# Kernel optimization log

Hardware: AMD Instinct MI355X
Metric: run time of the kernel (lower is better)

## Reference

```python
import jax, jax.numpy as jnp
import numpy as np

# Module hyperparameters (from init_kwargs)
B, D = 512, 65536        # input: [B, D]
Q = 64                   # sub-vectors per sample
R = 8                    # number of independent KMeans problems
L = 64                   # clusters (codebook size) per problem
ITERS = 10               # KMeans max_iter
SUBD = D // Q            # sub-vector dim = 1024
N = B * Q // R           # points per KMeans problem = 4096


def setup_inputs() -> dict:
    key = jax.random.key(0)
    x = jax.random.normal(key, (B, D), dtype=jnp.float32)
    return {"x": x}


def _kmeans(pts):
    """Batched Lloyd's KMeans. pts: [R, N, d]. Returns (labels [R,N], centers [R,L,d])."""
    # init: random distinct points per group (torch_kmeans 'rnd' init)
    key = jax.random.key(42)
    init_idx = jax.vmap(lambda k: jax.random.permutation(k, N)[:L])(
        jax.random.split(key, R))                          # [R, L]
    centers = jax.vmap(lambda p, i: p[i])(pts, init_idx)   # [R, L, d]
    x2 = jnp.sum(pts * pts, axis=-1, keepdims=True)        # [R, N, 1]

    def assign(centers):
        c2 = jnp.sum(centers * centers, axis=-1)           # [R, L]
        d2 = x2 + c2[:, None, :] - 2.0 * jnp.einsum('rnd,rld->rnl', pts, centers)
        return jnp.argmin(d2, axis=-1)                     # [R, N]

    def step(centers, _):
        labels = assign(centers)
        onehot = jax.nn.one_hot(labels, L, dtype=pts.dtype)      # [R, N, L]
        counts = jnp.sum(onehot, axis=1)                          # [R, L]
        sums = jnp.einsum('rnl,rnd->rld', onehot, pts)            # [R, L, d]
        new_c = jnp.where(counts[..., None] > 0,
                          sums / jnp.maximum(counts[..., None], 1.0),
                          centers)                                # keep empty clusters
        return new_c, None

    centers, _ = jax.lax.scan(step, centers, None, length=ITERS)
    labels = assign(centers)
    return labels, centers


def _quantize(x):
    orig_shape = x.shape
    pts = x.reshape(B, Q, SUBD).reshape(R, N, SUBD)        # [R, N, d/q]
    labels, centers = _kmeans(pts)
    # gather: replace each point by its centroid
    xq = jax.vmap(lambda c, lab: c[lab])(centers, labels)  # [R, N, d/q]
    return xq.reshape(orig_shape)


def reference(x):
    # FedLite_Layer.forward in training mode
    return _quantize(x)
```

## Files before the change

kernel.cpp:

```cpp
#include <hip/hip_runtime.h>
#include <stdint.h>
#include <stddef.h>


#define JAX_PARTITIONABLE 1

static constexpr int R_    = 8;
static constexpr int N_    = 4096;
static constexpr int L_    = 64;
static constexpr int D_    = 1024;
static constexpr int ITERS = 10;
static constexpr int ROWS  = R_ * N_;
static constexpr int SEGS  = 8;

__device__ __forceinline__ unsigned rotl32(unsigned x, int r) {
  return (x << r) | (x >> (32 - r));
}

__device__ __forceinline__ void tf2x32(unsigned k0, unsigned k1,
                                       unsigned c0, unsigned c1,
                                       unsigned &o0, unsigned &o1) {
  unsigned ks2 = k0 ^ k1 ^ 0x1BD11BDAu;
  unsigned x0 = c0 + k0, x1 = c1 + k1;
#define TF_R4(a,b,c,d) { x0 += x1; x1 = rotl32(x1,a); x1 ^= x0; \
                         x0 += x1; x1 = rotl32(x1,b); x1 ^= x0; \
                         x0 += x1; x1 = rotl32(x1,c); x1 ^= x0; \
                         x0 += x1; x1 = rotl32(x1,d); x1 ^= x0; }
  TF_R4(13,15,26,6);  x0 += k1;  x1 += ks2 + 1u;
  TF_R4(17,29,16,24); x0 += ks2; x1 += k0  + 2u;
  TF_R4(13,15,26,6);  x0 += k0;  x1 += k1  + 3u;
  TF_R4(17,29,16,24); x0 += k1;  x1 += ks2 + 4u;
  TF_R4(13,15,26,6);  x0 += ks2; x1 += k0  + 5u;
#undef TF_R4
  o0 = x0; o1 = x1;
}

__device__ __forceinline__ void jax_split2(unsigned k0, unsigned k1,
                                           unsigned &nk0, unsigned &nk1,
                                           unsigned &sk0, unsigned &sk1) {
#if JAX_PARTITIONABLE
  tf2x32(k0, k1, 0u, 0u, nk0, nk1);
  tf2x32(k0, k1, 0u, 1u, sk0, sk1);
#else
  unsigned a0, a1, b0, b1;
  tf2x32(k0, k1, 0u, 2u, a0, a1);
  tf2x32(k0, k1, 1u, 3u, b0, b1);
  nk0 = a0; nk1 = b0; sk0 = a1; sk1 = b1;
#endif
}

__global__ __launch_bounds__(1024) void k_rng_x2(const float* __restrict__ pts,
                                                 float* __restrict__ x2,
                                                 int* __restrict__ init_idx) {
  __shared__ unsigned long long arr[N_];
  __shared__ unsigned short perm[N_];
  const int t = threadIdx.x;

  if (blockIdx.x >= R_) {
    const int row = (blockIdx.x - R_) * 16 + (t >> 6);
    const int lane = t & 63;
    const float4* P = (const float4*)(pts + (size_t)row * D_);
    float s = 0.f;
#pragma unroll
    for (int i = 0; i < 4; ++i) {
      float4 v = P[lane + 64 * i];
      s += v.x * v.x + v.y * v.y + v.z * v.z + v.w * v.w;
    }
#pragma unroll
    for (int m = 32; m > 0; m >>= 1) s += __shfl_down(s, m);
    if (lane == 0) x2[row] = s;
    return;
  }

  const int r = blockIdx.x;

  unsigned k0, k1;
#if JAX_PARTITIONABLE
  tf2x32(0u, 42u, 0u, (unsigned)r, k0, k1);
#else
  {
    unsigned a0, a1, b0, b1;
    unsigned i0 = 2u * r, i1 = 2u * r + 1u;
    if (r < 4) { tf2x32(0u, 42u, i0, i0 + 8u, a0, a1); tf2x32(0u, 42u, i1, i1 + 8u, b0, b1); k0 = a0; k1 = b0; }
    else       { tf2x32(0u, 42u, i0 - 8u, i0, a0, a1); tf2x32(0u, 42u, i1 - 8u, i1, b0, b1); k0 = a1; k1 = b1; }
  }
#endif

  for (int i = t; i < N_; i += 1024) perm[i] = (unsigned short)i;
  __syncthreads();

  for (int round = 0; round < 2; ++round) {
    unsigned nk0, nk1, sk0, sk1;
    jax_split2(k0, k1, nk0, nk1, sk0, sk1);
    for (int j = t; j < N_; j += 1024) {
      unsigned o0, o1, skey;
#if JAX_PARTITIONABLE
      tf2x32(sk0, sk1, 0u, (unsigned)j, o0, o1);
      skey = o0 ^ o1;
#else
      if (j < 2048) { tf2x32(sk0, sk1, (unsigned)j, (unsigned)(j + 2048), o0, o1); skey = o0; }
      else          { tf2x32(sk0, sk1, (unsigned)(j - 2048), (unsigned)j, o0, o1); skey = o1; }
#endif
      arr[j] = ((unsigned long long)skey << 24) |
               ((unsigned long long)(unsigned)j << 12) |
               (unsigned long long)perm[j];
    }
    __syncthreads();
    for (int k = 2; k <= N_; k <<= 1) {
      for (int j2 = k >> 1; j2 >= 1; j2 >>= 1) {
        for (int q = t; q < N_ / 2; q += 1024) {
          int low = q & (j2 - 1);
          int i0 = ((q ^ low) << 1) | low;
          int i1 = i0 | j2;
          bool up = ((i0 & k) == 0);
          unsigned long long a = arr[i0], b = arr[i1];
          if ((a > b) == up) { arr[i0] = b; arr[i1] = a; }
        }
        __syncthreads();
      }
    }
    for (int j = t; j < N_; j += 1024) perm[j] = (unsigned short)(arr[j] & 0xFFFull);
    __syncthreads();
    k0 = nk0; k1 = nk1;
  }
  if (t < L_) init_idx[r * L_ + t] = (int)perm[t];
}

__global__ __launch_bounds__(256) void k_gather_init(const float* __restrict__ pts,
                                                     const int* __restrict__ init_idx,
                                                     float* __restrict__ centers,
                                                     float* __restrict__ c2,
                                                     int* __restrict__ counts) {
  const int l = blockIdx.x, r = blockIdx.y, t = threadIdx.x;
  const int idx = init_idx[r * L_ + l];
  const float4* src = (const float4*)(pts + ((size_t)r * N_ + idx) * D_);
  float4* dst = (float4*)(centers + ((size_t)r * L_ + l) * D_);
  float4 v = src[t];
  dst[t] = v;
  float s = v.x * v.x + v.y * v.y + v.z * v.z + v.w * v.w;
  __shared__ float red[4];
  const int lane = t & 63, wave = t >> 6;
#pragma unroll
  for (int m = 32; m > 0; m >>= 1) s += __shfl_down(s, m);
  if (lane == 0) red[wave] = s;
  __syncthreads();
  if (t == 0) {
    c2[r * L_ + l] = red[0] + red[1] + red[2] + red[3];
    counts[r * L_ + l] = 0;
  }
}

#define BN 128
#define BK 64
__global__ __launch_bounds__(256, 1) void k_assign(const float* __restrict__ pts,
                                                   const float* __restrict__ centers,
                                                   const float* __restrict__ c2g,
                                                   const float* __restrict__ x2g,
                                                   int* __restrict__ labels,
                                                   int* __restrict__ counts) {
  __shared__ __align__(16) float pT[2][BK][BN + 4];
  __shared__ __align__(16) float cL[2][L_][BK + 4];
  __shared__ int hist[L_];
  const int t = threadIdx.x;
  const int r = blockIdx.y;
  const int n0 = blockIdx.x * BN;
  const int lane = t & 63;
  const int w  = t >> 6;
  const int u  = lane & 3;
  const int qq = lane >> 2;
  const int p0 = (w * 4 + u) * 8;
  const int l0 = qq * 4;

  const float* Pr = pts + ((size_t)r * N_ + n0) * D_;
  const float* Cr = centers + (size_t)r * L_ * D_;

  const int srow = t >> 4;
  const int skk  = (t & 15) * 4;
  const int swz  = 4 * (t & 7);
  const int crow = t >> 2;
  const int cseg = (t & 3) * 16;

  if (t < L_) hist[t] = 0;

  float4 pv4[8], cv4[4];

#pragma unroll
  for (int i = 0; i < 8; ++i)
    pv4[i] = *(const float4*)(Pr + (size_t)(i * 16 + srow) * D_ + skk);
#pragma unroll
  for (int c = 0; c < 4; ++c)
    cv4[c] = *(const float4*)(Cr + (size_t)crow * D_ + cseg + 4 * c);
#pragma unroll
  for (int i = 0; i < 8; ++i) {
    const int col = (i * 16 + srow) ^ swz;
    pT[0][skk + 0][col] = pv4[i].x;
    pT[0][skk + 1][col] = pv4[i].y;
    pT[0][skk + 2][col] = pv4[i].z;
    pT[0][skk + 3][col] = pv4[i].w;
  }
#pragma unroll
  for (int c = 0; c < 4; ++c)
    *(float4*)&cL[0][crow][cseg + 4 * c] = cv4[c];
  __syncthreads();

  float acc[8][4];
#pragma unroll
  for (int i = 0; i < 8; ++i)
#pragma unroll
    for (int j = 0; j < 4; ++j) acc[i][j] = 0.f;

  constexpr int NKB = D_ / BK;
  for (int kb = 0; kb < NKB; ++kb) {
    const int cur = kb & 1;
    if (kb + 1 < NKB) {
      const int kbase = (kb + 1) * BK;
#pragma unroll
      for (int i = 0; i < 8; ++i)
        pv4[i] = *(const float4*)(Pr + (size_t)(i * 16 + srow) * D_ + kbase + skk);
#pragma unroll
      for (int c = 0; c < 4; ++c)
        cv4[c] = *(const float4*)(Cr + (size_t)crow * D_ + kbase + cseg + 4 * c);
    }

#pragma unroll 4
    for (int kk4 = 0; kk4 < 16; ++kk4) {
      const int sig4 = 4 * (kk4 & 7);
      const int colA = p0 ^ sig4;
      const float4 cq = *(const float4*)&cL[cur][lane][kk4 * 4];
      const float ca[4] = {cq.x, cq.y, cq.z, cq.w};
#pragma unroll
      for (int e = 0; e < 4; ++e) {
        const int kk = kk4 * 4 + e;
        const float4 A = *(const float4*)&pT[cur][kk][colA];
        const float4 B = *(const float4*)&pT[cur][kk][colA ^ 4];
        const int ci = __float_as_int(ca[e]);
        const float cb0 = __int_as_float(__builtin_amdgcn_mov_dpp(ci, 0x00, 0xF, 0xF, true));
        const float cb1 = __int_as_float(__builtin_amdgcn_mov_dpp(ci, 0x55, 0xF, 0xF, true));
        const float cb2 = __int_as_float(__builtin_amdgcn_mov_dpp(ci, 0xAA, 0xF, 0xF, true));
        const float cb3 = __int_as_float(__builtin_amdgcn_mov_dpp(ci, 0xFF, 0xF, 0xF, true));
        const float pv[8] = {A.x, A.y, A.z, A.w, B.x, B.y, B.z, B.w};
#pragma unroll
        for (int i = 0; i < 8; ++i) {
          acc[i][0] = fmaf(pv[i], cb0, acc[i][0]);
          acc[i][1] = fmaf(pv[i], cb1, acc[i][1]);
          acc[i][2] = fmaf(pv[i], cb2, acc[i][2]);
          acc[i][3] = fmaf(pv[i], cb3, acc[i][3]);
        }
      }
    }

    if (kb + 1 < NKB) {
      const int nxt = cur ^ 1;
#pragma unroll
      for (int i = 0; i < 8; ++i) {
        const int col = (i * 16 + srow) ^ swz;
        pT[nxt][skk + 0][col] = pv4[i].x;
        pT[nxt][skk + 1][col] = pv4[i].y;
        pT[nxt][skk + 2][col] = pv4[i].z;
        pT[nxt][skk + 3][col] = pv4[i].w;
      }
#pragma unroll
      for (int c = 0; c < 4; ++c)
        *(float4*)&cL[nxt][crow][cseg + 4 * c] = cv4[c];
    }
    __syncthreads();
  }

  float c2v[4];
#pragma unroll
  for (int j = 0; j < 4; ++j) c2v[j] = c2g[r * L_ + l0 + j];

#pragma unroll
  for (int i = 0; i < 8; ++i) {
    const int n = n0 + p0 + i;
    const float x2i = x2g[r * N_ + n];
    float bv = 3.4e38f;
    int bi = 0;
#pragma unroll
    for (int j = 0; j < 4; ++j) {
      float d2 = (x2i + c2v[j]) - 2.0f * acc[i][j];
      if (d2 < bv) { bv = d2; bi = l0 + j; }
    }
#pragma unroll
    for (int m = 4; m <= 32; m <<= 1) {
      float ov = __shfl_xor(bv, m);
      int oi = __shfl_xor(bi, m);
      if (ov < bv || (ov == bv && oi < bi)) { bv = ov; bi = oi; }
    }
    if (qq == 0) {
      labels[r * N_ + n] = bi;
      atomicAdd(&hist[bi], 1);
    }
  }
  __syncthreads();
  if (t < L_) atomicAdd(&counts[r * L_ + t], hist[t]);
}

__global__ __launch_bounds__(256) void k_update(const float* __restrict__ pts,
                                                const int* __restrict__ labels,
                                                float* __restrict__ psums) {
  __shared__ float acc[L_ * 256];
  __shared__ int lab[512];
  const int dch = blockIdx.x;
  const int seg = blockIdx.y;
  const int r   = blockIdx.z;
  const int t = threadIdx.x;

  for (int i = t; i < L_ * 256; i += 256) acc[i] = 0.f;
  for (int i = t; i < 512; i += 256) lab[i] = labels[r * N_ + seg * 512 + i];
  __syncthreads();

  const float* P = pts + ((size_t)r * N_ + seg * 512) * D_ + dch * 256 + t;
  float vbuf[8];
#pragma unroll
  for (int w = 0; w < 8; ++w) vbuf[w] = P[(size_t)w * D_];
  for (int nb = 0; nb < 504; nb += 8) {
#pragma unroll
    for (int w = 0; w < 8; ++w) {
      const int n = nb + w;
      const float cur = vbuf[w];
      vbuf[w] = P[(size_t)(n + 8) * D_];
      acc[lab[n] * 256 + t] += cur;
    }
  }
#pragma unroll
  for (int w = 0; w < 8; ++w) acc[lab[504 + w] * 256 + t] += vbuf[w];
  __syncthreads();

  float* S = psums + (((size_t)r * SEGS + seg) * L_) * D_ + dch * 256;
  for (int i = t; i < L_ * 256; i += 256) {
    int l = i >> 8, dd = i & 255;
    S[(size_t)l * D_ + dd] = acc[i];
  }
}

__global__ __launch_bounds__(256) void k_reduce(const float* __restrict__ psums,
                                                int* __restrict__ counts,
                                                float* __restrict__ centers,
                                                float* __restrict__ c2) {
  const int l = blockIdx.x, r = blockIdx.y, t = threadIdx.x;
  const int cnt = counts[r * L_ + l];
  const float denom = fmaxf((float)cnt, 1.0f);

  float4 s = {0.f, 0.f, 0.f, 0.f};
#pragma unroll
  for (int seg = 0; seg < SEGS; ++seg) {
    const float4 v = *(const float4*)(psums + (((size_t)r * SEGS + seg) * L_ + l) * D_ + t * 4);
    s.x += v.x; s.y += v.y; s.z += v.z; s.w += v.w;
  }
  float4* Crow = (float4*)(centers + ((size_t)r * L_ + l) * D_);
  float4 cn;
  if (cnt > 0) {
    cn.x = s.x / denom; cn.y = s.y / denom; cn.z = s.z / denom; cn.w = s.w / denom;
  } else {
    cn = Crow[t];
  }
  Crow[t] = cn;

  float ssq = cn.x * cn.x + cn.y * cn.y + cn.z * cn.z + cn.w * cn.w;
  __shared__ float red[4];
  const int lane = t & 63, wave = t >> 6;
#pragma unroll
  for (int m = 32; m > 0; m >>= 1) ssq += __shfl_down(ssq, m);
  if (lane == 0) red[wave] = ssq;
  __syncthreads();
  if (t == 0) {
    c2[r * L_ + l] = red[0] + red[1] + red[2] + red[3];
    counts[r * L_ + l] = 0;
  }
}

__global__ __launch_bounds__(256) void k_final(const float* __restrict__ centers,
                                               const int* __restrict__ labels,
                                               float* __restrict__ out) {
  const int t = threadIdx.x;
  const int row = blockIdx.x * 4 + (t >> 6);
  const int lane = t & 63;
  const int r = row >> 12;
  const int lab = labels[row];
  const float4* src = (const float4*)(centers + ((size_t)r * L_ + lab) * D_);
  float4* dst = (float4*)(out + (size_t)row * D_);
#pragma unroll
  for (int i = 0; i < 4; ++i) dst[lane + 64 * i] = src[lane + 64 * i];
}

extern "C" void kernel_launch(void* const* d_in, const int* in_sizes, int n_in,
                              void* d_out, int out_size, void* d_ws, size_t ws_size,
                              hipStream_t stream) {
  const float* x = (const float*)d_in[0];
  float* out = (float*)d_out;
  char* ws = (char*)d_ws;

  float* centers = (float*)(ws + 0);
  float* c2      = (float*)(ws + 2097152);
  float* x2      = (float*)(ws + 2099200);
  int*   labels  = (int*)  (ws + 2230272);
  int*   counts  = (int*)  (ws + 2361344);
  int*   initidx = (int*)  (ws + 2363392);
  float* psums   = (float*)(ws + 2365440);
  (void)in_sizes; (void)n_in; (void)out_size; (void)ws_size;

  k_rng_x2<<<dim3(R_ + ROWS / 16), 1024, 0, stream>>>(x, x2, initidx);
  k_gather_init<<<dim3(L_, R_), 256, 0, stream>>>(x, initidx, centers, c2, counts);

  for (int it = 0; it < ITERS; ++it) {
    k_assign<<<dim3(N_ / BN, R_), 256, 0, stream>>>(x, centers, c2, x2, labels, counts);
    k_update<<<dim3(4, SEGS, R_), 256, 0, stream>>>(x, labels, psums);
    k_reduce<<<dim3(L_, R_), 256, 0, stream>>>(psums, counts, centers, c2);
  }
  k_assign<<<dim3(N_ / BN, R_), 256, 0, stream>>>(x, centers, c2, x2, labels, counts);
  k_final<<<dim3(ROWS / 4), 256, 0, stream>>>(centers, labels, out);
}
```

Measured before the change: 1.786 ms.

## Shrink assign tile to 64 points and split update into 128-thread blocks

The assign kernel's point tile drops from 128 to 64 rows, with a 4x4 per-thread accumulator and a merged center/point load pattern. This doubles the grid to 512 blocks and allows two blocks per CU, giving more parallelism across the device's CUs. The update kernel now uses 128-thread blocks covering 128 columns, doubling its grid and halving shared memory per block. The cost is lower arithmetic intensity: centers are reloaded for every 64 points instead of every 128.

```diff
diff --git a/kernel.cpp b/kernel.cpp
--- a/kernel.cpp
+++ b/kernel.cpp
@@ -150,9 +150,9 @@
   }
 }
 
-#define BN 128
+#define BN 64
 #define BK 64
-__global__ __launch_bounds__(256, 1) void k_assign(const float* __restrict__ pts,
+__global__ __launch_bounds__(256, 2) void k_assign(const float* __restrict__ pts,
                                                    const float* __restrict__ centers,
                                                    const float* __restrict__ c2g,
                                                    const float* __restrict__ x2g,
@@ -168,7 +168,7 @@
   const int w  = t >> 6;
   const int u  = lane & 3;
   const int qq = lane >> 2;
-  const int p0 = (w * 4 + u) * 8;
+  const int p0 = w * 16 + u * 4;
   const int l0 = qq * 4;
 
   const float* Pr = pts + ((size_t)r * N_ + n0) * D_;
@@ -177,35 +177,31 @@
   const int srow = t >> 4;
   const int skk  = (t & 15) * 4;
   const int swz  = 4 * (t & 7);
-  const int crow = t >> 2;
-  const int cseg = (t & 3) * 16;
 
   if (t < L_) hist[t] = 0;
 
-  float4 pv4[8], cv4[4];
-
-#pragma unroll
-  for (int i = 0; i < 8; ++i)
+  float4 pv4[4], cv4[4];
+
+#pragma unroll
+  for (int i = 0; i < 4; ++i) {
     pv4[i] = *(const float4*)(Pr + (size_t)(i * 16 + srow) * D_ + skk);
-#pragma unroll
-  for (int c = 0; c < 4; ++c)
-    cv4[c] = *(const float4*)(Cr + (size_t)crow * D_ + cseg + 4 * c);
-#pragma unroll
-  for (int i = 0; i < 8; ++i) {
-    const int col = (i * 16 + srow) ^ swz;
+    cv4[i] = *(const float4*)(Cr + (size_t)(i * 16 + srow) * D_ + skk);
+  }
+#pragma unroll
+  for (int i = 0; i < 4; ++i) {
+    const int row = i * 16 + srow;
+    const int col = row ^ swz;
     pT[0][skk + 0][col] = pv4[i].x;
     pT[0][skk + 1][col] = pv4[i].y;
     pT[0][skk + 2][col] = pv4[i].z;
     pT[0][skk + 3][col] = pv4[i].w;
-  }
-#pragma unroll
-  for (int c = 0; c < 4; ++c)
-    *(float4*)&cL[0][crow][cseg + 4 * c] = cv4[c];
-  __syncthreads();
-
-  float acc[8][4];
-#pragma unroll
-  for (int i = 0; i < 8; ++i)
+    *(float4*)&cL[0][row][skk] = cv4[i];
+  }
+  __syncthreads();
+
+  float acc[4][4];
+#pragma unroll
+  for (int i = 0; i < 4; ++i)
 #pragma unroll
     for (int j = 0; j < 4; ++j) acc[i][j] = 0.f;
 
@@ -215,11 +211,10 @@
     if (kb + 1 < NKB) {
       const int kbase = (kb + 1) * BK;
 #pragma unroll
-      for (int i = 0; i < 8; ++i)
+      for (int i = 0; i < 4; ++i) {
         pv4[i] = *(const float4*)(Pr + (size_t)(i * 16 + srow) * D_ + kbase + skk);
-#pragma unroll
-      for (int c = 0; c < 4; ++c)
-        cv4[c] = *(const float4*)(Cr + (size_t)crow * D_ + kbase + cseg + 4 * c);
+        cv4[i] = *(const float4*)(Cr + (size_t)(i * 16 + srow) * D_ + kbase + skk);
+      }
     }
 
 #pragma unroll 4
@@ -232,15 +227,14 @@
       for (int e = 0; e < 4; ++e) {
         const int kk = kk4 * 4 + e;
         const float4 A = *(const float4*)&pT[cur][kk][colA];
-        const float4 B = *(const float4*)&pT[cur][kk][colA ^ 4];
         const int ci = __float_as_int(ca[e]);
         const float cb0 = __int_as_float(__builtin_amdgcn_mov_dpp(ci, 0x00, 0xF, 0xF, true));
         const float cb1 = __int_as_float(__builtin_amdgcn_mov_dpp(ci, 0x55, 0xF, 0xF, true));
         const float cb2 = __int_as_float(__builtin_amdgcn_mov_dpp(ci, 0xAA, 0xF, 0xF, true));
         const float cb3 = __int_as_float(__builtin_amdgcn_mov_dpp(ci, 0xFF, 0xF, 0xF, true));
-        const float pv[8] = {A.x, A.y, A.z, A.w, B.x, B.y, B.z, B.w};
-#pragma unroll
-        for (int i = 0; i < 8; ++i) {
+        const float pv[4] = {A.x, A.y, A.z, A.w};
+#pragma unroll
+        for (int i = 0; i < 4; ++i) {
           acc[i][0] = fmaf(pv[i], cb0, acc[i][0]);
           acc[i][1] = fmaf(pv[i], cb1, acc[i][1]);
           acc[i][2] = fmaf(pv[i], cb2, acc[i][2]);
@@ -252,16 +246,15 @@
     if (kb + 1 < NKB) {
       const int nxt = cur ^ 1;
 #pragma unroll
-      for (int i = 0; i < 8; ++i) {
-        const int col = (i * 16 + srow) ^ swz;
+      for (int i = 0; i < 4; ++i) {
+        const int row = i * 16 + srow;
+        const int col = row ^ swz;
         pT[nxt][skk + 0][col] = pv4[i].x;
         pT[nxt][skk + 1][col] = pv4[i].y;
         pT[nxt][skk + 2][col] = pv4[i].z;
         pT[nxt][skk + 3][col] = pv4[i].w;
+        *(float4*)&cL[nxt][row][skk] = cv4[i];
       }
-#pragma unroll
-      for (int c = 0; c < 4; ++c)
-        *(float4*)&cL[nxt][crow][cseg + 4 * c] = cv4[c];
     }
     __syncthreads();
   }
@@ -271,7 +264,7 @@
   for (int j = 0; j < 4; ++j) c2v[j] = c2g[r * L_ + l0 + j];
 
 #pragma unroll
-  for (int i = 0; i < 8; ++i) {
+  for (int i = 0; i < 4; ++i) {
     const int n = n0 + p0 + i;
     const float x2i = x2g[r * N_ + n];
     float bv = 3.4e38f;
@@ -296,21 +289,21 @@
   if (t < L_) atomicAdd(&counts[r * L_ + t], hist[t]);
 }
 
-__global__ __launch_bounds__(256) void k_update(const float* __restrict__ pts,
-                                                const int* __restrict__ labels,
-                                                float* __restrict__ psums) {
-  __shared__ float acc[L_ * 256];
+__global__ __launch_bounds__(128, 2) void k_update(const float* __restrict__ pts,
+                                                   const int* __restrict__ labels,
+                                                   float* __restrict__ psums) {
+  __shared__ float acc[L_ * 128];
   __shared__ int lab[512];
   const int dch = blockIdx.x;
   const int seg = blockIdx.y;
   const int r   = blockIdx.z;
   const int t = threadIdx.x;
 
-  for (int i = t; i < L_ * 256; i += 256) acc[i] = 0.f;
-  for (int i = t; i < 512; i += 256) lab[i] = labels[r * N_ + seg * 512 + i];
-  __syncthreads();
-
-  const float* P = pts + ((size_t)r * N_ + seg * 512) * D_ + dch * 256 + t;
+  for (int i = t; i < L_ * 128; i += 128) acc[i] = 0.f;
+  for (int i = t; i < 512; i += 128) lab[i] = labels[r * N_ + seg * 512 + i];
+  __syncthreads();
+
+  const float* P = pts + ((size_t)r * N_ + seg * 512) * D_ + dch * 128 + t;
   float vbuf[8];
 #pragma unroll
   for (int w = 0; w < 8; ++w) vbuf[w] = P[(size_t)w * D_];
@@ -320,16 +313,16 @@
       const int n = nb + w;
       const float cur = vbuf[w];
       vbuf[w] = P[(size_t)(n + 8) * D_];
-      acc[lab[n] * 256 + t] += cur;
-    }
-  }
-#pragma unroll
-  for (int w = 0; w < 8; ++w) acc[lab[504 + w] * 256 + t] += vbuf[w];
-  __syncthreads();
-
-  float* S = psums + (((size_t)r * SEGS + seg) * L_) * D_ + dch * 256;
-  for (int i = t; i < L_ * 256; i += 256) {
-    int l = i >> 8, dd = i & 255;
+      acc[lab[n] * 128 + t] += cur;
+    }
+  }
+#pragma unroll
+  for (int w = 0; w < 8; ++w) acc[lab[504 + w] * 128 + t] += vbuf[w];
+  __syncthreads();
+
+  float* S = psums + (((size_t)r * SEGS + seg) * L_) * D_ + dch * 128;
+  for (int i = t; i < L_ * 128; i += 128) {
+    int l = i >> 7, dd = i & 127;
     S[(size_t)l * D_ + dd] = acc[i];
   }
 }
@@ -405,7 +398,7 @@
 
   for (int it = 0; it < ITERS; ++it) {
     k_assign<<<dim3(N_ / BN, R_), 256, 0, stream>>>(x, centers, c2, x2, labels, counts);
-    k_update<<<dim3(4, SEGS, R_), 256, 0, stream>>>(x, labels, psums);
+    k_update<<<dim3(8, SEGS, R_), 128, 0, stream>>>(x, labels, psums);
     k_reduce<<<dim3(L_, R_), 256, 0, stream>>>(psums, counts, centers, c2);
   }
   k_assign<<<dim3(N_ / BN, R_), 256, 0, stream>>>(x, centers, c2, x2, labels, counts);
```

After: 1.536 ms. -14.0%, faster.
